# Kernel optimization log

Measured on AMD Instinct MI355X. Metric: run time of the kernel, lower is better.

Reference implementation:

```python
import jax, jax.numpy as jnp
import numpy as np

CC = 0.25        # commitment_cost
BN_EPS = 1e-5    # BatchNorm1d eps (eval mode, running_mean=0, running_var=1)
EPS_PPL = 1e-10


def _res_block(x, W1, b1, W2, b2, gamma, beta):
    # Linear(D,16) -> ReLU -> Linear(16,D) -> ReLU -> BatchNorm1d(eval), residual add
    h = jax.nn.relu(x @ W1 + b1)
    h = jax.nn.relu(h @ W2 + b2)
    h = h / jnp.sqrt(1.0 + BN_EPS) * gamma + beta
    return x + h


def setup_inputs() -> dict:
    B, IN, L1, D, ED, K = 512, 4096, 2048, 512, 64, 512
    key = jax.random.key(0)
    ks = iter(jax.random.split(key, 48))

    def rn(shape, s=0.02):
        return (jax.random.normal(next(ks), shape) * s).astype(jnp.float32)

    z = lambda *s: jnp.zeros(s, jnp.float32)
    inp = {
        "x": jax.random.normal(next(ks), (B, IN), dtype=jnp.float32),
        # encoder
        "We1": rn((IN, L1)), "be1": z(L1),
        "We2": rn((L1, D)), "be2": z(D),
        "Wre1": rn((D, 16)), "bre1": z(16), "Wre2": rn((16, D)), "bre2": z(D),
        "ge": jnp.ones((D,), jnp.float32), "bebn": z(D),
        # VQ
        "E": jax.random.uniform(next(ks), (K, ED), jnp.float32, -1.0 / K, 1.0 / K),
        "Wt1": rn((1, ED // 2)), "bt1": z(ED // 2),
        "Wt2": rn((ED // 2, ED)), "bt2": z(ED),
        "Wc": rn((ED * D, 10)), "bc": z(10),
        # decoder
        "Wp": rn((ED * D, D)), "bp": z(D),
        "Wrd1": rn((D, 16)), "brd1": z(16), "Wrd2": rn((16, D)), "brd2": z(D),
        "gd": jnp.ones((D,), jnp.float32), "bdbn": z(D),
        "Wd1": rn((D, L1)), "bd1": z(L1),
        "Wd2": rn((L1, IN)), "bd2": z(IN),
    }
    return inp


def reference(x, We1, be1, We2, be2, Wre1, bre1, Wre2, bre2, ge, bebn,
              E, Wt1, bt1, Wt2, bt2, Wc, bc,
              Wp, bp, Wrd1, brd1, Wrd2, brd2, gd, bdbn, Wd1, bd1, Wd2, bd2):
    # ---- Encoder (dropout = identity in eval) ----
    h = jax.nn.relu(x @ We1 + be1)          # [B, enc_lay1]
    zenc = jax.nn.relu(h @ We2 + be2)       # [B, enc_dim]
    zenc = _res_block(zenc, Wre1, bre1, Wre2, bre2, ge, bebn)

    # ---- VectorQuantizer ----
    B, D = zenc.shape
    e = jax.nn.relu(zenc[..., None] @ Wt1 + bt1) @ Wt2 + bt2   # [B, D, ED]
    ED = e.shape[-1]
    K = E.shape[0]
    flat = e.reshape(-1, ED)                                    # [(B*D), ED]
    dist = (jnp.sum(flat * flat, axis=1, keepdims=True)
            + jnp.sum(E * E, axis=1)
            - 2.0 * flat @ E.T)                                 # [(B*D), K]
    idx = jnp.argmin(dist, axis=1)                              # [(B*D)]
    q = E[idx].reshape(B, D, ED)                                # gather == onehot @ E
    counts = jnp.zeros((K,), flat.dtype).at[idx].add(1.0) / idx.shape[0]

    cls = jax.nn.sigmoid(q.reshape(B, D * ED) @ Wc + bc)        # [B, 10]

    e_loss = jnp.mean((jax.lax.stop_gradient(q) - e) ** 2)
    q_loss = jnp.mean((q - jax.lax.stop_gradient(e)) ** 2)
    vq_loss = q_loss + CC * e_loss

    q_st = (e + jax.lax.stop_gradient(q - e)).reshape(B, D * ED)  # straight-through
    p = jax.lax.stop_gradient(counts)
    perplexity = jnp.exp(-jnp.sum(p * jnp.log(p + EPS_PPL)))

    # ---- Decoder ----
    d = jax.nn.relu(q_st @ Wp + bp)
    d = _res_block(d, Wrd1, brd1, Wrd2, brd2, gd, bdbn)
    d = jax.nn.relu(d @ Wd1 + bd1)
    x_recon = jax.nn.relu(d @ Wd2 + bd2)
    return (vq_loss, x_recon, perplexity, q_st, cls, zenc)
```

## Files before the change

kernel.cpp:

```cpp
#include <hip/hip_runtime.h>

typedef unsigned int uint;

enum { ACT_RELU=0, ACT_SIGMOID=1, ACT_RESBN=2 };

template<int ACT>
__global__ __launch_bounds__(256) void gemm_fused(
    const float* __restrict__ A, const float* __restrict__ W,
    const float* __restrict__ bias, float* __restrict__ C,
    float* __restrict__ C2, const float* __restrict__ R,
    const float* __restrict__ gamma, const float* __restrict__ beta,
    int M, int N, int K)
{
    __shared__ float As[16][68];
    __shared__ float Bs[16][68];
    const int tx = threadIdx.x, ty = threadIdx.y;
    const int tid = ty*16 + tx;
    const int row0 = blockIdx.y*64, col0 = blockIdx.x*64;
    float acc[4][4] = {};
    for (int k0 = 0; k0 < K; k0 += 16) {
        #pragma unroll
        for (int t = tid; t < 1024; t += 256) {
            int r = t >> 4, c = t & 15;
            As[c][r] = A[(size_t)(row0+r)*K + k0 + c];
        }
        #pragma unroll
        for (int t = tid; t < 1024; t += 256) {
            int kr = t >> 6, c = t & 63;
            int gc = col0 + c;
            Bs[kr][c] = (gc < N) ? W[(size_t)(k0+kr)*N + gc] : 0.f;
        }
        __syncthreads();
        #pragma unroll
        for (int kk = 0; kk < 16; kk++) {
            float a[4], b[4];
            #pragma unroll
            for (int i = 0; i < 4; i++) a[i] = As[kk][ty*4+i];
            #pragma unroll
            for (int j = 0; j < 4; j++) b[j] = Bs[kk][tx*4+j];
            #pragma unroll
            for (int i = 0; i < 4; i++)
                #pragma unroll
                for (int j = 0; j < 4; j++)
                    acc[i][j] += a[i]*b[j];
        }
        __syncthreads();
    }
    const float INVS = 0.99999500003749968f;
    #pragma unroll
    for (int i = 0; i < 4; i++) {
        int r = row0 + ty*4 + i;
        #pragma unroll
        for (int j = 0; j < 4; j++) {
            int c = col0 + tx*4 + j;
            if (c < N) {
                float v = acc[i][j] + bias[c];
                if (ACT == ACT_RELU) {
                    v = fmaxf(v, 0.f);
                } else if (ACT == ACT_SIGMOID) {
                    v = 1.f/(1.f + expf(-v));
                } else {
                    v = fmaxf(v, 0.f);
                    v = v*(gamma[c]*INVS) + beta[c];
                    v += R[(size_t)r*N + c];
                }
                C[(size_t)r*N + c] = v;
                if (C2) C2[(size_t)r*N + c] = v;
            }
        }
    }
}

__global__ __launch_bounds__(256) void gemm_acc(
    const float* __restrict__ A, const float* __restrict__ W,
    float* __restrict__ C, int M, int N, int K, int kchunk)
{
    __shared__ float As[16][68];
    __shared__ float Bs[16][68];
    const int tx = threadIdx.x, ty = threadIdx.y;
    const int tid = ty*16 + tx;
    const int row0 = blockIdx.y*64, col0 = blockIdx.x*64;
    const int kbeg = blockIdx.z * kchunk, kend = kbeg + kchunk;
    float acc[4][4] = {};
    for (int k0 = kbeg; k0 < kend; k0 += 16) {
        #pragma unroll
        for (int t = tid; t < 1024; t += 256) {
            int r = t >> 4, c = t & 15;
            As[c][r] = A[(size_t)(row0+r)*K + k0 + c];
        }
        #pragma unroll
        for (int t = tid; t < 1024; t += 256) {
            int kr = t >> 6, c = t & 63;
            int gc = col0 + c;
            Bs[kr][c] = (gc < N) ? W[(size_t)(k0+kr)*N + gc] : 0.f;
        }
        __syncthreads();
        #pragma unroll
        for (int kk = 0; kk < 16; kk++) {
            float a[4], b[4];
            #pragma unroll
            for (int i = 0; i < 4; i++) a[i] = As[kk][ty*4+i];
            #pragma unroll
            for (int j = 0; j < 4; j++) b[j] = Bs[kk][tx*4+j];
            #pragma unroll
            for (int i = 0; i < 4; i++)
                #pragma unroll
                for (int j = 0; j < 4; j++)
                    acc[i][j] += a[i]*b[j];
        }
        __syncthreads();
    }
    #pragma unroll
    for (int i = 0; i < 4; i++) {
        int r = row0 + ty*4 + i;
        #pragma unroll
        for (int j = 0; j < 4; j++) {
            int c = col0 + tx*4 + j;
            if (c < N) atomicAdd(&C[(size_t)r*N + c], acc[i][j]);
        }
    }
}

__device__ inline float4 ld4_a8(const float* p) {
    float2 lo = *(const float2*)p;
    float2 hi = *(const float2*)(p + 2);
    return make_float4(lo.x, lo.y, hi.x, hi.y);
}

template<bool A16>
__global__ __launch_bounds__(256)
__attribute__((amdgpu_waves_per_eu(2, 4)))
void gemm_big(
    const float* __restrict__ A, const float* __restrict__ W,
    float* __restrict__ C, int M, int N, int K, int kchunk)
{
    __shared__ float As[16][132];
    __shared__ float Bs[16][132];
    const int tid = threadIdx.x;
    const int tx = tid & 15, ty = tid >> 4;
    const int row0 = blockIdx.y*128, col0 = blockIdx.x*128;
    const size_t kbeg = (size_t)blockIdx.z * kchunk;

    const int ar0 = tid >> 2;
    const int ac0 = (tid & 3) * 4;
    const int ar1 = ar0 + 64;
    const int bk0 = tid >> 5;
    const int bc0 = (tid & 31) * 4;
    const int bk1 = bk0 + 8;

    const float* Ap0 = A + (size_t)(row0 + ar0)*K + kbeg + ac0;
    const float* Ap1 = A + (size_t)(row0 + ar1)*K + kbeg + ac0;
    const float* Bp0 = W + (kbeg + bk0)*(size_t)N + col0 + bc0;
    const float* Bp1 = W + (kbeg + bk1)*(size_t)N + col0 + bc0;

    float4 pa0 = A16 ? *(const float4*)Ap0 : ld4_a8(Ap0);
    float4 pa1 = A16 ? *(const float4*)Ap1 : ld4_a8(Ap1);
    float4 pb0 = *(const float4*)Bp0;
    float4 pb1 = *(const float4*)Bp1;

    float acc[8][8] = {};

    for (int k0 = 0; k0 < kchunk; k0 += 16) {
        As[ac0+0][ar0] = pa0.x; As[ac0+1][ar0] = pa0.y;
        As[ac0+2][ar0] = pa0.z; As[ac0+3][ar0] = pa0.w;
        As[ac0+0][ar1] = pa1.x; As[ac0+1][ar1] = pa1.y;
        As[ac0+2][ar1] = pa1.z; As[ac0+3][ar1] = pa1.w;
        *(float4*)&Bs[bk0][bc0] = pb0;
        *(float4*)&Bs[bk1][bc0] = pb1;
        __syncthreads();
        if (k0 + 16 < kchunk) {
            pa0 = A16 ? *(const float4*)(Ap0 + k0 + 16) : ld4_a8(Ap0 + k0 + 16);
            pa1 = A16 ? *(const float4*)(Ap1 + k0 + 16) : ld4_a8(Ap1 + k0 + 16);
            pb0 = *(const float4*)(Bp0 + (size_t)(k0+16)*N);
            pb1 = *(const float4*)(Bp1 + (size_t)(k0+16)*N);
        }
        #pragma unroll
        for (int kk = 0; kk < 16; kk++) {
            float a[8], b[8];
            *(float4*)&a[0] = *(const float4*)&As[kk][ty*8];
            *(float4*)&a[4] = *(const float4*)&As[kk][ty*8+4];
            *(float4*)&b[0] = *(const float4*)&Bs[kk][tx*8];
            *(float4*)&b[4] = *(const float4*)&Bs[kk][tx*8+4];
            #pragma unroll
            for (int i = 0; i < 8; i++)
                #pragma unroll
                for (int j = 0; j < 8; j++)
                    acc[i][j] += a[i]*b[j];
        }
        __syncthreads();
    }

    #pragma unroll
    for (int i = 0; i < 8; i++) {
        float* crow = C + (size_t)(row0 + ty*8 + i)*N + col0 + tx*8;
        #pragma unroll
        for (int j = 0; j < 8; j++)
            atomicAdd(crow + j, acc[i][j]);
    }
}

template<int ACT>
__global__ __launch_bounds__(256) void epi_k(
    float* __restrict__ C, const float* __restrict__ bias,
    float* __restrict__ dst, int M, int N)
{
    int i = blockIdx.x*256 + threadIdx.x;
    if (i >= M*N) return;
    int c = i % N;
    float v = C[i] + bias[c];
    if (ACT == ACT_RELU) v = fmaxf(v, 0.f);
    else v = 1.f/(1.f + expf(-v));
    C[i] = v;
    if (dst) dst[i] = v;
}

__global__ __launch_bounds__(256) void zero_k(float* __restrict__ p, int n)
{
    int i = blockIdx.x*256 + threadIdx.x;
    if (i < n) p[i] = 0.f;
}

__global__ __launch_bounds__(256) void esq2_k(
    const float* __restrict__ E, const float* __restrict__ bt2,
    const float* __restrict__ Wt2,
    float* __restrict__ C2, float* __restrict__ Hm2)
{
    int k = blockIdx.x*256 + threadIdx.x;
    if (k >= 512) return;
    const float4* Er = (const float4*)(E + (size_t)k*64);
    const float4* b4 = (const float4*)bt2;
    float esq = 0.f, g0 = 0.f;
    #pragma unroll
    for (int m = 0; m < 16; m++) {
        float4 w = Er[m]; float4 b = b4[m];
        esq += w.x*w.x + w.y*w.y + w.z*w.z + w.w*w.w;
        g0  += b.x*w.x + b.y*w.y + b.z*w.z + b.w*w.w;
    }
    C2[k] = esq - 2.f*g0;
    for (int i = 0; i < 32; i++) {
        const float4* Wr = (const float4*)(Wt2 + i*64);
        float h = 0.f;
        #pragma unroll
        for (int m = 0; m < 16; m++) {
            float4 w = Er[m]; float4 ww = Wr[m];
            h += w.x*ww.x + w.y*ww.y + w.z*ww.z + w.w*ww.w;
        }
        Hm2[(size_t)k*32 + i] = -2.f*h;
    }
}

__global__ __launch_bounds__(256) void vqc_k(
    const float* __restrict__ zencf, const float* __restrict__ Wt1,
    const float* __restrict__ bt1, const float* __restrict__ bt2,
    const float* __restrict__ Wt2, const float* __restrict__ E,
    const float* __restrict__ C2, const float* __restrict__ Hm2,
    float* __restrict__ qout, float* __restrict__ hist,
    float* __restrict__ sspart)
{
    __shared__ float aT[32][256];
    __shared__ int   rowbi[256];
    __shared__ int   hcnt[512];
    __shared__ float red4[4];
    const int tid = threadIdx.x;
    const int gid = blockIdx.x*256 + tid;
    const float z = zencf[gid];

    hcnt[tid] = 0; hcnt[tid + 256] = 0;

    float a[32];
    #pragma unroll
    for (int i = 0; i < 32; i++) {
        a[i] = fmaxf(z*Wt1[i] + bt1[i], 0.f);
        aT[i][tid] = a[i];
    }
    __syncthreads();

    float best = 3.4e38f; int bi = 0;
    for (int k = 0; k < 512; k++) {
        const float* hp = Hm2 + k*32;
        float s = C2[k];
        #pragma unroll
        for (int i = 0; i < 32; i++) s = fmaf(a[i], hp[i], s);
        if (s < best) { best = s; bi = k; }
    }
    atomicAdd(&hcnt[bi], 1);
    rowbi[tid] = bi;

    float ls = 0.f;
    const float4* Eq = (const float4*)(E + (size_t)bi*64);
    const float4* b4 = (const float4*)bt2;
    for (int m = 0; m < 16; m++) {
        float4 w = Eq[m];
        float4 e4 = b4[m];
        #pragma unroll 8
        for (int i = 0; i < 32; i++) {
            float ai = aT[i][tid];
            float4 wr = *(const float4*)(Wt2 + i*64 + 4*m);
            e4.x = fmaf(ai, wr.x, e4.x);
            e4.y = fmaf(ai, wr.y, e4.y);
            e4.z = fmaf(ai, wr.z, e4.z);
            e4.w = fmaf(ai, wr.w, e4.w);
        }
        float d;
        d = w.x - e4.x; ls += d*d;
        d = w.y - e4.y; ls += d*d;
        d = w.z - e4.z; ls += d*d;
        d = w.w - e4.w; ls += d*d;
    }
    #pragma unroll
    for (int off = 32; off > 0; off >>= 1)
        ls += __shfl_down(ls, off, 64);
    if ((tid & 63) == 0) red4[tid >> 6] = ls;

    __syncthreads();

    if (tid == 0)
        sspart[blockIdx.x] = ((red4[0] + red4[1]) + red4[2]) + red4[3];
    hist[(size_t)blockIdx.x*512 + tid]       = (float)hcnt[tid];
    hist[(size_t)blockIdx.x*512 + 256 + tid] = (float)hcnt[tid + 256];

    const int wid  = tid >> 6;
    const int lane = tid & 63;
    float2* qo2w = (float2*)qout + ((size_t)blockIdx.x*8192 + (size_t)wid*2048);
    const int rbase = wid*64;
    #pragma unroll 4
    for (int c = 0; c < 32; c++) {
        const int idx2 = c*64 + lane;
        const int r    = rbase + (idx2 >> 5);
        const int d2   = idx2 & 31;
        const int bir  = rowbi[r];
        float2 w2 = *((const float2*)(E + (size_t)bir*64) + d2);
        qo2w[idx2] = w2;
    }
}

__global__ __launch_bounds__(512) void finalize_k(
    const float* __restrict__ hist, const float* __restrict__ sspart,
    float* __restrict__ out)
{
    __shared__ float red[512];
    int tid = threadIdx.x;
    float c = 0.f;
    for (int b = 0; b < 1024; b++) c += hist[(size_t)b*512 + tid];
    red[tid] = sspart[tid] + sspart[tid + 512];
    __syncthreads();
    for (int s = 256; s > 0; s >>= 1) { if (tid < s) red[tid] += red[tid+s]; __syncthreads(); }
    float ss = red[0];
    __syncthreads();
    float p = c * (1.f/262144.f);
    red[tid] = p * logf(p + 1e-10f);
    __syncthreads();
    for (int s = 256; s > 0; s >>= 1) { if (tid < s) red[tid] += red[tid+s]; __syncthreads(); }
    if (tid == 0) {
        out[0]       = 1.25f * ss * (1.f/16777216.f);
        out[2097153] = expf(-red[0]);
    }
}

extern "C" void kernel_launch(void* const* d_in, const int* in_sizes, int n_in,
                              void* d_out, int out_size, void* d_ws, size_t ws_size,
                              hipStream_t stream)
{
    const float* x    = (const float*)d_in[0];
    const float* We1  = (const float*)d_in[1];  const float* be1  = (const float*)d_in[2];
    const float* We2  = (const float*)d_in[3];  const float* be2  = (const float*)d_in[4];
    const float* Wre1 = (const float*)d_in[5];  const float* bre1 = (const float*)d_in[6];
    const float* Wre2 = (const float*)d_in[7];  const float* bre2 = (const float*)d_in[8];
    const float* ge   = (const float*)d_in[9];  const float* bebn = (const float*)d_in[10];
    const float* E    = (const float*)d_in[11];
    const float* Wt1  = (const float*)d_in[12]; const float* bt1  = (const float*)d_in[13];
    const float* Wt2  = (const float*)d_in[14]; const float* bt2  = (const float*)d_in[15];
    const float* Wc   = (const float*)d_in[16]; const float* bc   = (const float*)d_in[17];
    const float* Wp   = (const float*)d_in[18]; const float* bp   = (const float*)d_in[19];
    const float* Wrd1 = (const float*)d_in[20]; const float* brd1 = (const float*)d_in[21];
    const float* Wrd2 = (const float*)d_in[22]; const float* brd2 = (const float*)d_in[23];
    const float* gd   = (const float*)d_in[24]; const float* bdbn = (const float*)d_in[25];
    const float* Wd1  = (const float*)d_in[26]; const float* bd1  = (const float*)d_in[27];
    const float* Wd2  = (const float*)d_in[28]; const float* bd2  = (const float*)d_in[29];

    float* out    = (float*)d_out;
    float* o_xr   = out + 1;
    float* o_q    = out + 2097154;
    float* o_cls  = out + 18874370;
    float* o_zenc = out + 18879490;

    float* ws    = (float*)d_ws;
    float* t1    = ws + 528;
    float* t2    = ws + 8720;
    float* clsf  = ws + 16912;
    float* z0    = ws + 22032;
    float* dp0   = ws + 284176;
    float* zencf = ws + 546320;
    float* dd    = ws + 808464;
    float* hbuf  = ws + 1070608;
    float* d2    = ws + 1070608;
    float* c2t   = ws + 1070608;
    float* hm2t  = ws + 1071120;
    float* hist  = ws + 1087504;
    float* sspart= ws + 1611792;

    dim3 blk(16, 16);

    zero_k<<<dim3(2135), dim3(256), 0, stream>>>(ws, 546320);
    zero_k<<<dim3(4096), dim3(256), 0, stream>>>(hbuf, 1048576);
    zero_k<<<dim3(8192), dim3(256), 0, stream>>>(o_xr, 2097152);

    gemm_big<true><<<dim3(16, 4, 8), dim3(256), 0, stream>>>(
        x, We1, hbuf, 512, 2048, 4096, 512);
    epi_k<ACT_RELU><<<dim3(4096), dim3(256), 0, stream>>>(hbuf, be1, nullptr, 512, 2048);
    gemm_big<true><<<dim3(4, 4, 32), dim3(256), 0, stream>>>(
        hbuf, We2, z0, 512, 512, 2048, 64);
    epi_k<ACT_RELU><<<dim3(1024), dim3(256), 0, stream>>>(z0, be2, nullptr, 512, 512);
    gemm_acc<<<dim3(1, 8, 32), blk, 0, stream>>>(z0, Wre1, t1, 512, 16, 512, 16);
    epi_k<ACT_RELU><<<dim3(32), dim3(256), 0, stream>>>(t1, bre1, nullptr, 512, 16);
    gemm_fused<ACT_RESBN><<<dim3(8, 8), blk, 0, stream>>>(
        t1, Wre2, bre2, zencf, o_zenc, z0, ge, bebn, 512, 512, 16);

    esq2_k<<<dim3(2), dim3(256), 0, stream>>>(E, bt2, Wt2, c2t, hm2t);
    vqc_k<<<dim3(1024), dim3(256), 0, stream>>>(zencf, Wt1, bt1, bt2, Wt2, E,
                                                c2t, hm2t, o_q, hist, sspart);
    finalize_k<<<dim3(1), dim3(512), 0, stream>>>(hist, sspart, out);

    gemm_acc<<<dim3(1, 8, 32), blk, 0, stream>>>(o_q, Wc, clsf, 512, 10, 32768, 1024);
    epi_k<ACT_SIGMOID><<<dim3(20), dim3(256), 0, stream>>>(clsf, bc, o_cls, 512, 10);

    gemm_big<false><<<dim3(4, 4, 32), dim3(256), 0, stream>>>(
        o_q, Wp, dp0, 512, 512, 32768, 1024);
    epi_k<ACT_RELU><<<dim3(1024), dim3(256), 0, stream>>>(dp0, bp, nullptr, 512, 512);
    gemm_acc<<<dim3(1, 8, 32), blk, 0, stream>>>(dp0, Wrd1, t2, 512, 16, 512, 16);
    epi_k<ACT_RELU><<<dim3(32), dim3(256), 0, stream>>>(t2, brd1, nullptr, 512, 16);
    gemm_fused<ACT_RESBN><<<dim3(8, 8), blk, 0, stream>>>(
        t2, Wrd2, brd2, dd, nullptr, dp0, gd, bdbn, 512, 512, 16);
    zero_k<<<dim3(4096), dim3(256), 0, stream>>>(d2, 1048576);
    gemm_big<true><<<dim3(16, 4, 8), dim3(256), 0, stream>>>(
        dd, Wd1, d2, 512, 2048, 512, 64);
    epi_k<ACT_RELU><<<dim3(4096), dim3(256), 0, stream>>>(d2, bd1, nullptr, 512, 2048);
    gemm_big<true><<<dim3(32, 4, 4), dim3(256), 0, stream>>>(
        d2, Wd2, o_xr, 512, 4096, 2048, 512);
    epi_k<ACT_RELU><<<dim3(8192), dim3(256), 0, stream>>>(o_xr, bd2, nullptr, 512, 4096);
}
```

Baseline: 2.387 ms.

## Double-buffer shared tiles in gemm_big and split B column reads

Converts the big split-K GEMM to double-buffered LDS tiles, so the next tile is stored into the alternate buffer after compute and only one barrier is needed per iteration instead of two. It also changes each thread's B/C column mapping from eight contiguous columns to two groups of four (tx*4 and 64+tx*4), which is meant to reduce LDS bank conflicts on the B reads and to make the atomic adds more contiguous across threads. The cost is double the shared memory, which may reduce occupancy.

```diff
diff --git a/kernel.cpp b/kernel.cpp
--- a/kernel.cpp
+++ b/kernel.cpp
@@ -134,8 +134,8 @@
     const float* __restrict__ A, const float* __restrict__ W,
     float* __restrict__ C, int M, int N, int K, int kchunk)
 {
-    __shared__ float As[16][132];
-    __shared__ float Bs[16][132];
+    __shared__ float As[2][16][132];
+    __shared__ float Bs[2][16][132];
     const int tid = threadIdx.x;
     const int tx = tid & 15, ty = tid >> 4;
     const int row0 = blockIdx.y*128, col0 = blockIdx.x*128;
@@ -153,49 +153,67 @@
     const float* Bp0 = W + (kbeg + bk0)*(size_t)N + col0 + bc0;
     const float* Bp1 = W + (kbeg + bk1)*(size_t)N + col0 + bc0;
 
-    float4 pa0 = A16 ? *(const float4*)Ap0 : ld4_a8(Ap0);
-    float4 pa1 = A16 ? *(const float4*)Ap1 : ld4_a8(Ap1);
-    float4 pb0 = *(const float4*)Bp0;
-    float4 pb1 = *(const float4*)Bp1;
+    {
+        float4 a0 = A16 ? *(const float4*)Ap0 : ld4_a8(Ap0);
+        float4 a1 = A16 ? *(const float4*)Ap1 : ld4_a8(Ap1);
+        float4 b0 = *(const float4*)Bp0;
+        float4 b1 = *(const float4*)Bp1;
+        As[0][ac0+0][ar0] = a0.x; As[0][ac0+1][ar0] = a0.y;
+        As[0][ac0+2][ar0] = a0.z; As[0][ac0+3][ar0] = a0.w;
+        As[0][ac0+0][ar1] = a1.x; As[0][ac0+1][ar1] = a1.y;
+        As[0][ac0+2][ar1] = a1.z; As[0][ac0+3][ar1] = a1.w;
+        *(float4*)&Bs[0][bk0][bc0] = b0;
+        *(float4*)&Bs[0][bk1][bc0] = b1;
+    }
+    __syncthreads();
 
     float acc[8][8] = {};
-
-    for (int k0 = 0; k0 < kchunk; k0 += 16) {
-        As[ac0+0][ar0] = pa0.x; As[ac0+1][ar0] = pa0.y;
-        As[ac0+2][ar0] = pa0.z; As[ac0+3][ar0] = pa0.w;
-        As[ac0+0][ar1] = pa1.x; As[ac0+1][ar1] = pa1.y;
-        As[ac0+2][ar1] = pa1.z; As[ac0+3][ar1] = pa1.w;
-        *(float4*)&Bs[bk0][bc0] = pb0;
-        *(float4*)&Bs[bk1][bc0] = pb1;
-        __syncthreads();
-        if (k0 + 16 < kchunk) {
-            pa0 = A16 ? *(const float4*)(Ap0 + k0 + 16) : ld4_a8(Ap0 + k0 + 16);
-            pa1 = A16 ? *(const float4*)(Ap1 + k0 + 16) : ld4_a8(Ap1 + k0 + 16);
-            pb0 = *(const float4*)(Bp0 + (size_t)(k0+16)*N);
-            pb1 = *(const float4*)(Bp1 + (size_t)(k0+16)*N);
+    const int nt = kchunk >> 4;
+
+    for (int t = 0; t < nt; t++) {
+        const int cur = t & 1, nxt = cur ^ 1;
+        float4 pa0, pa1, pb0, pb1;
+        const bool more = (t + 1 < nt);
+        if (more) {
+            const int off = (t + 1) << 4;
+            pa0 = A16 ? *(const float4*)(Ap0 + off) : ld4_a8(Ap0 + off);
+            pa1 = A16 ? *(const float4*)(Ap1 + off) : ld4_a8(Ap1 + off);
+            pb0 = *(const float4*)(Bp0 + (size_t)off*N);
+            pb1 = *(const float4*)(Bp1 + (size_t)off*N);
         }
         #pragma unroll
         for (int kk = 0; kk < 16; kk++) {
             float a[8], b[8];
-            *(float4*)&a[0] = *(const float4*)&As[kk][ty*8];
-            *(float4*)&a[4] = *(const float4*)&As[kk][ty*8+4];
-            *(float4*)&b[0] = *(const float4*)&Bs[kk][tx*8];
-            *(float4*)&b[4] = *(const float4*)&Bs[kk][tx*8+4];
+            *(float4*)&a[0] = *(const float4*)&As[cur][kk][ty*8];
+            *(float4*)&a[4] = *(const float4*)&As[cur][kk][ty*8+4];
+            *(float4*)&b[0] = *(const float4*)&Bs[cur][kk][tx*4];
+            *(float4*)&b[4] = *(const float4*)&Bs[cur][kk][64 + tx*4];
             #pragma unroll
             for (int i = 0; i < 8; i++)
                 #pragma unroll
                 for (int j = 0; j < 8; j++)
                     acc[i][j] += a[i]*b[j];
         }
+        if (more) {
+            As[nxt][ac0+0][ar0] = pa0.x; As[nxt][ac0+1][ar0] = pa0.y;
+            As[nxt][ac0+2][ar0] = pa0.z; As[nxt][ac0+3][ar0] = pa0.w;
+            As[nxt][ac0+0][ar1] = pa1.x; As[nxt][ac0+1][ar1] = pa1.y;
+            As[nxt][ac0+2][ar1] = pa1.z; As[nxt][ac0+3][ar1] = pa1.w;
+            *(float4*)&Bs[nxt][bk0][bc0] = pb0;
+            *(float4*)&Bs[nxt][bk1][bc0] = pb1;
+        }
         __syncthreads();
     }
 
     #pragma unroll
     for (int i = 0; i < 8; i++) {
-        float* crow = C + (size_t)(row0 + ty*8 + i)*N + col0 + tx*8;
-        #pragma unroll
-        for (int j = 0; j < 8; j++)
-            atomicAdd(crow + j, acc[i][j]);
+        float* crow = C + (size_t)(row0 + ty*8 + i)*N + col0;
+        #pragma unroll
+        for (int j = 0; j < 4; j++)
+            atomicAdd(crow + tx*4 + j, acc[i][j]);
+        #pragma unroll
+        for (int j = 0; j < 4; j++)
+            atomicAdd(crow + 64 + tx*4 + j, acc[i][4+j]);
     }
 }
 
```

After: 3.894 ms. +63.1%, slower.
